# Optimization experiments

Hardware: AMD Instinct MI355X
Metric: run time of the kernel (lower is better)

Reference implementation:

```python
import jax, jax.numpy as jnp
import numpy as np
import math

B, S, D, H = 4, 2048, 1024, 16
DK = D // H


def setup_inputs() -> dict:
    key = jax.random.key(0)
    ks = jax.random.split(key, 12)
    scale = 1.0 / math.sqrt(D)
    inp = {
        "x": jax.random.normal(ks[0], (B, S, D), jnp.float32),
        "q": jax.random.normal(ks[1], (B, S, D), jnp.float32),
        "k": jax.random.normal(ks[2], (B, S, D), jnp.float32),
        "v": jax.random.normal(ks[3], (B, S, D), jnp.float32),
        # causal mask: 1 = keep, 0 = masked
        "mask": jnp.tril(jnp.ones((S, S), jnp.int32))[None, None],
        "wq": jax.random.normal(ks[4], (D, D), jnp.float32) * scale,
        "bq": jnp.zeros((D,), jnp.float32),
        "wk": jax.random.normal(ks[5], (D, D), jnp.float32) * scale,
        "bk": jnp.zeros((D,), jnp.float32),
        "wv": jax.random.normal(ks[6], (D, D), jnp.float32) * scale,
        "bv": jnp.zeros((D,), jnp.float32),
        "wo": jax.random.normal(ks[7], (D, D), jnp.float32) * scale,
        "bo": jnp.zeros((D,), jnp.float32),
    }
    return inp


def _split_heads(t):  # [B,S,D] -> [B,H,S,DK]
    return t.reshape(B, S, H, DK).transpose(0, 2, 1, 3)


def reference(x, q, k, v, mask, wq, bq, wk, bk, wv, bv, wo, bo):
    # x is accepted for signature parity with the torch module but is
    # overwritten inside the original forward; it does not affect output.
    query = _split_heads(q @ wq + bq)
    key_h = _split_heads(k @ wk + bk)
    value = _split_heads(v @ wv + bv)
    # scores: [B,H,Sq,Sk]
    scores = jnp.einsum("bhqd,bhkd->bhqk", query, key_h) / math.sqrt(DK)
    scores = jnp.where(mask == 0, jnp.float32(-1e9), scores)
    attn = jax.nn.softmax(scores, axis=-1)  # dropout p=0.0 -> identity
    out = jnp.einsum("bhqk,bhkd->bhqd", attn, value)
    out = out.transpose(0, 2, 1, 3).reshape(B, S, D)
    return out @ wo + bo
```

## Files before the change

kernel.cpp:

```cpp
#include <hip/hip_runtime.h>

typedef unsigned short u16;
typedef __bf16 bf16x8 __attribute__((ext_vector_type(8)));
typedef float f32x4 __attribute__((ext_vector_type(4)));
typedef u16 u16x8 __attribute__((ext_vector_type(8)));
typedef u16 u16x4 __attribute__((ext_vector_type(4)));

static constexpr int Bb = 4, Ss = 2048, Dd = 1024, Hh = 16, DKk = 64;
static constexpr int Mg = Bb * Ss;
static constexpr int Kg = Dd;
static constexpr int Ng = Dd;

#if __has_builtin(__builtin_amdgcn_exp2f)
#define EXP2 __builtin_amdgcn_exp2f
#else
#define EXP2 exp2f
#endif

__device__ __forceinline__ u16 f2b(float f) {
    union { __bf16 h; u16 u; } c; c.h = (__bf16)f; return c.u;
}

typedef const __attribute__((address_space(1))) void gas_t;
typedef __attribute__((address_space(3))) void las_t;
__device__ __forceinline__ void gll16(const void* g, void* l) {
    __builtin_amdgcn_global_load_lds((gas_t*)g, (las_t*)l, 16, 0, 0);
}

__global__ __launch_bounds__(256) void wt4_kernel(const float* w0, const float* w1,
                                                  const float* w2, const float* w3,
                                                  u16* t0, u16* t1, u16* t2, u16* t3) {
    const float* W; u16* Wt;
    switch (blockIdx.z) {
        case 0: W = w0; Wt = t0; break;
        case 1: W = w1; Wt = t1; break;
        case 2: W = w2; Wt = t2; break;
        default: W = w3; Wt = t3; break;
    }
    __shared__ __attribute__((aligned(16))) u16 T[64 * 72];
    const int k0 = blockIdx.x * 64, n0 = blockIdx.y * 64;
    const int tid = threadIdx.x;
    for (int i = 0; i < 4; ++i) {
        int flat = tid + i * 256;
        int r = flat >> 4, c4 = flat & 15;
        float4 w4 = *(const float4*)(W + (size_t)(k0 + r) * 1024 + n0 + c4 * 4);
        u16* d = &T[r * 72 + c4 * 4];
        d[0] = f2b(w4.x); d[1] = f2b(w4.y); d[2] = f2b(w4.z); d[3] = f2b(w4.w);
    }
    __syncthreads();
    for (int i = 0; i < 2; ++i) {
        int flat = tid + i * 256;
        int n = flat >> 3, c8 = flat & 7;
        u16x8 v;
        for (int jj = 0; jj < 8; ++jj) v[jj] = T[(c8 * 8 + jj) * 72 + n];
        *(u16x8*)(Wt + (size_t)(n0 + n) * 1024 + k0 + c8 * 8) = v;
    }
}

__global__ __launch_bounds__(256) void qkv_gemm(
    const float* __restrict__ qin, const float* __restrict__ kin,
    const float* __restrict__ vin,
    const u16* __restrict__ WqT, const u16* __restrict__ WkT,
    const u16* __restrict__ WvT,
    const float* __restrict__ bq, const float* __restrict__ bk,
    const float* __restrict__ bv,
    u16* __restrict__ Qw, u16* __restrict__ Kw, u16* __restrict__ VwT,
    float qscale) {
    __shared__ __attribute__((aligned(16))) u16 As[128 * 32];
    __shared__ __attribute__((aligned(16))) u16 Bs[128 * 32];
    const int z = blockIdx.z;
    const float* A = (z == 0) ? qin : (z == 1) ? kin : vin;
    const u16* Bt = (z == 0) ? WqT : (z == 1) ? WkT : WvT;
    const float* bias = (z == 0) ? bq : (z == 1) ? bk : bv;
    const float scale = (z == 0) ? qscale : 1.0f;

    const int tid = threadIdx.x;
    const int wave = tid >> 6, lane = tid & 63;
    const int quad = lane >> 4, l15 = lane & 15;
    const int m0 = blockIdx.x * 128, n0 = blockIdx.y * 128;
    const int wm = (wave >> 1) * 64, wn = (wave & 1) * 64;
    const int rr = lane >> 2, cc = (lane & 3) * 8;

    const u16* Bg = Bt + (size_t)(n0 + wave * 32 + rr) * Kg + cc;
    u16* Bsw = &Bs[wave * 32 * 32];

    f32x4 acc[4][4] = {};

    for (int k0 = 0; k0 < Kg; k0 += 32) {
        __syncthreads();
        gll16(Bg + k0, Bsw);
        gll16(Bg + k0 + (size_t)16 * Kg, Bsw + 16 * 32);
        for (int i = 0; i < 4; ++i) {
            int flat = tid + i * 256;
            int r = flat >> 3, c4 = flat & 7;
            float4 a4 = *(const float4*)(A + (size_t)(m0 + r) * Kg + k0 + c4 * 4);
            u16x4 pk;
            pk[0] = f2b(a4.x); pk[1] = f2b(a4.y); pk[2] = f2b(a4.z); pk[3] = f2b(a4.w);
            *(u16x4*)(&As[r * 32 + c4 * 4]) = pk;
        }
        __syncthreads();

        bf16x8 a[4], b[4];
        for (int i = 0; i < 4; ++i)
            a[i] = *(const bf16x8*)(&As[(wm + i * 16 + l15) * 32 + quad * 8]);
        for (int j = 0; j < 4; ++j)
            b[j] = *(const bf16x8*)(&Bs[(wn + j * 16 + l15) * 32 + quad * 8]);
        if (z < 2) {
            for (int i = 0; i < 4; ++i)
                for (int j = 0; j < 4; ++j)
                    acc[i][j] = __builtin_amdgcn_mfma_f32_16x16x32_bf16(b[j], a[i], acc[i][j], 0, 0, 0);
        } else {
            for (int i = 0; i < 4; ++i)
                for (int j = 0; j < 4; ++j)
                    acc[i][j] = __builtin_amdgcn_mfma_f32_16x16x32_bf16(a[i], b[j], acc[i][j], 0, 0, 0);
        }
    }

    if (z < 2) {
        u16* Out = (z == 0) ? Qw : Kw;
        for (int i = 0; i < 4; ++i) {
            int m_row = m0 + wm + i * 16 + l15;
            int bb = m_row >> 11, s = m_row & 2047;
            for (int j = 0; j < 4; ++j) {
                int nb = n0 + wn + j * 16 + quad * 4;
                float4 b4 = *(const float4*)(bias + nb);
                int h = nb >> 6, dk = nb & 63;
                u16x4 pk;
                pk[0] = f2b((acc[i][j][0] + b4.x) * scale);
                pk[1] = f2b((acc[i][j][1] + b4.y) * scale);
                pk[2] = f2b((acc[i][j][2] + b4.z) * scale);
                pk[3] = f2b((acc[i][j][3] + b4.w) * scale);
                *(u16x4*)(Out + (((size_t)bb * Hh + h) * Ss + s) * DKk + dk) = pk;
            }
        }
    } else {
        for (int i = 0; i < 4; ++i) {
            for (int j = 0; j < 4; ++j) {
                int col = n0 + wn + j * 16 + l15;
                float bvv = bias[col];
                int h = col >> 6, dk = col & 63;
                int row0 = m0 + wm + i * 16 + quad * 4;
                int bb = row0 >> 11, s0 = row0 & 2047;
                u16x4 pk;
                for (int r = 0; r < 4; ++r) pk[r] = f2b(acc[i][j][r] + bvv);
                *(u16x4*)(VwT + (((size_t)bb * Hh + h) * DKk + dk) * Ss + s0) = pk;
            }
        }
    }
}

__global__ __launch_bounds__(256) void out_gemm(const u16* __restrict__ A,
                                                const u16* __restrict__ Bt,
                                                const float* __restrict__ bias,
                                                float* __restrict__ Out) {
    __shared__ __attribute__((aligned(16))) u16 As[128 * 32];
    __shared__ __attribute__((aligned(16))) u16 Bs[128 * 32];
    const int tid = threadIdx.x;
    const int wave = tid >> 6, lane = tid & 63;
    const int quad = lane >> 4, l15 = lane & 15;
    const int m0 = blockIdx.x * 128, n0 = blockIdx.y * 128;
    const int wm = (wave >> 1) * 64, wn = (wave & 1) * 64;
    const int rr = lane >> 2, cc = (lane & 3) * 8;

    const u16* Ag = A + (size_t)(m0 + wave * 32 + rr) * Kg + cc;
    const u16* Bg = Bt + (size_t)(n0 + wave * 32 + rr) * Kg + cc;
    u16* Asw = &As[wave * 32 * 32];
    u16* Bsw = &Bs[wave * 32 * 32];

    f32x4 acc[4][4] = {};

    for (int k0 = 0; k0 < Kg; k0 += 32) {
        __syncthreads();
        gll16(Ag + k0, Asw);
        gll16(Ag + k0 + (size_t)16 * Kg, Asw + 16 * 32);
        gll16(Bg + k0, Bsw);
        gll16(Bg + k0 + (size_t)16 * Kg, Bsw + 16 * 32);
        __syncthreads();

        bf16x8 a[4], b[4];
        for (int i = 0; i < 4; ++i)
            a[i] = *(const bf16x8*)(&As[(wm + i * 16 + l15) * 32 + quad * 8]);
        for (int j = 0; j < 4; ++j)
            b[j] = *(const bf16x8*)(&Bs[(wn + j * 16 + l15) * 32 + quad * 8]);
        for (int i = 0; i < 4; ++i)
            for (int j = 0; j < 4; ++j)
                acc[i][j] = __builtin_amdgcn_mfma_f32_16x16x32_bf16(b[j], a[i], acc[i][j], 0, 0, 0);
    }

    for (int i = 0; i < 4; ++i) {
        int m_row = m0 + wm + i * 16 + l15;
        for (int j = 0; j < 4; ++j) {
            int nb = n0 + wn + j * 16 + quad * 4;
            float4 b4 = *(const float4*)(bias + nb);
            float4 o;
            o.x = acc[i][j][0] + b4.x;
            o.y = acc[i][j][1] + b4.y;
            o.z = acc[i][j][2] + b4.z;
            o.w = acc[i][j][3] + b4.w;
            *(float4*)(Out + (size_t)m_row * Ng + nb) = o;
        }
    }
}

__device__ __forceinline__ void tile_step(const u16* Ks, const u16* Vs, u16* Pw,
                                          bf16x8 aq0, bf16x8 aq1, int qrow,
                                          bool diag, int jbase, int quad, int l15,
                                          f32x4 (&acc_o)[4], float& l_r) {
    f32x4 sacc[4];
    for (int ct = 0; ct < 4; ++ct) {
        bf16x8 bk0 = *(const bf16x8*)(&Ks[(ct * 16 + l15) * 32 + quad * 8]);
        bf16x8 bk1 = *(const bf16x8*)(&Ks[2048 + (ct * 16 + l15) * 32 + quad * 8]);
        f32x4 z = {};
        z = __builtin_amdgcn_mfma_f32_16x16x32_bf16(bk0, aq0, z, 0, 0, 0);
        z = __builtin_amdgcn_mfma_f32_16x16x32_bf16(bk1, aq1, z, 0, 0, 0);
        sacc[ct] = z;
    }
    if (diag) {
        for (int ct = 0; ct < 4; ++ct) {
            int kbase = jbase + ct * 16 + quad * 4;
            for (int r = 0; r < 4; ++r)
                if (kbase + r > qrow) sacc[ct][r] = -1e30f;
        }
    }
    const float M0 = 8.0f;
    float sum = 0.f;
    for (int ct = 0; ct < 4; ++ct)
        for (int r = 0; r < 4; ++r) {
            float p = EXP2(sacc[ct][r] - M0);
            sacc[ct][r] = p;
            sum += p;
        }
    l_r += sum;
    for (int ct = 0; ct < 4; ++ct) {
        u16x4 pk;
        for (int r = 0; r < 4; ++r) pk[r] = f2b(sacc[ct][r]);
        *(u16x4*)(&Pw[l15 * 72 + ct * 16 + quad * 4]) = pk;
    }
    for (int sc = 0; sc < 2; ++sc) {
        bf16x8 ap = *(const bf16x8*)(&Pw[l15 * 72 + sc * 32 + quad * 8]);
        for (int dt = 0; dt < 4; ++dt) {
            bf16x8 bv = *(const bf16x8*)(&Vs[sc * 2048 + (dt * 16 + l15) * 32 + quad * 8]);
            acc_o[dt] = __builtin_amdgcn_mfma_f32_16x16x32_bf16(bv, ap, acc_o[dt], 0, 0, 0);
        }
    }
}

__global__ __launch_bounds__(256) void attn_kernel(const u16* __restrict__ Qw,
                                                   const u16* __restrict__ Kw,
                                                   const u16* __restrict__ Vt,
                                                   u16* __restrict__ Ow) {
    __shared__ __attribute__((aligned(16))) u16 QPs[4608];
    __shared__ __attribute__((aligned(16))) u16 Ks[4096];
    __shared__ __attribute__((aligned(16))) u16 Vs[4096];

    const int pi = blockIdx.x;
    const int bh = blockIdx.y;
    const int qt_lo = pi, qt_hi = (Ss / 64 - 1) - pi;
    const int tid = threadIdx.x, wave = tid >> 6, lane = tid & 63;
    const int quad = lane >> 4, l15 = lane & 15;
    const int rr = lane >> 2, cc = (lane & 3) * 8;

    const u16* Qb = Qw + (size_t)bh * Ss * DKk;
    const u16* Kb = Kw + (size_t)bh * Ss * DKk;
    const u16* Vb = Vt + (size_t)bh * DKk * Ss;

    for (int kc = 0; kc < 2; ++kc)
        gll16(Qb + (size_t)(qt_hi * 64 + wave * 16 + rr) * DKk + kc * 32 + cc,
              &QPs[kc * 2048 + wave * 16 * 32]);
    __syncthreads();
    bf16x8 aqh0 = *(const bf16x8*)(&QPs[(wave * 16 + l15) * 32 + quad * 8]);
    bf16x8 aqh1 = *(const bf16x8*)(&QPs[2048 + (wave * 16 + l15) * 32 + quad * 8]);
    __syncthreads();
    for (int kc = 0; kc < 2; ++kc)
        gll16(Qb + (size_t)(qt_lo * 64 + wave * 16 + rr) * DKk + kc * 32 + cc,
              &QPs[kc * 2048 + wave * 16 * 32]);
    __syncthreads();
    bf16x8 aql0 = *(const bf16x8*)(&QPs[(wave * 16 + l15) * 32 + quad * 8]);
    bf16x8 aql1 = *(const bf16x8*)(&QPs[2048 + (wave * 16 + l15) * 32 + quad * 8]);

    f32x4 oh[4] = {}, ol[4] = {};
    float lh = 0.f, ll = 0.f;
    const int qrow_hi = qt_hi * 64 + wave * 16 + l15;
    const int qrow_lo = qt_lo * 64 + wave * 16 + l15;
    u16* Pw = &QPs[wave * 1152];

    for (int j = 0; j <= qt_hi; ++j) {
        __syncthreads();
        for (int c = 0; c < 2; ++c) {
            gll16(Kb + (size_t)(j * 64 + wave * 16 + rr) * DKk + c * 32 + cc,
                  &Ks[c * 2048 + wave * 16 * 32]);
            gll16(Vb + (size_t)(wave * 16 + rr) * Ss + j * 64 + c * 32 + cc,
                  &Vs[c * 2048 + wave * 16 * 32]);
        }
        __syncthreads();

        tile_step(Ks, Vs, Pw, aqh0, aqh1, qrow_hi, j == qt_hi, j * 64, quad, l15, oh, lh);
        if (j <= qt_lo)
            tile_step(Ks, Vs, Pw, aql0, aql1, qrow_lo, j == qt_lo, j * 64, quad, l15, ol, ll);
    }

    const int b = bh >> 4, h = bh & 15;
    {
        float L = lh;
        L += __shfl_xor(L, 16, 64);
        L += __shfl_xor(L, 32, 64);
        float inv = 1.f / L;
        int s = qt_hi * 64 + wave * 16 + l15;
        u16* orow = Ow + (((size_t)b * Ss + s) * Hh + h) * DKk;
        for (int dt = 0; dt < 4; ++dt) {
            u16x4 pk;
            for (int r = 0; r < 4; ++r) pk[r] = f2b(oh[dt][r] * inv);
            *(u16x4*)(orow + dt * 16 + quad * 4) = pk;
        }
    }
    {
        float L = ll;
        L += __shfl_xor(L, 16, 64);
        L += __shfl_xor(L, 32, 64);
        float inv = 1.f / L;
        int s = qt_lo * 64 + wave * 16 + l15;
        u16* orow = Ow + (((size_t)b * Ss + s) * Hh + h) * DKk;
        for (int dt = 0; dt < 4; ++dt) {
            u16x4 pk;
            for (int r = 0; r < 4; ++r) pk[r] = f2b(ol[dt][r] * inv);
            *(u16x4*)(orow + dt * 16 + quad * 4) = pk;
        }
    }
}

extern "C" void kernel_launch(void* const* d_in, const int* in_sizes, int n_in,
                              void* d_out, int out_size, void* d_ws, size_t ws_size,
                              hipStream_t stream) {
    const float* q  = (const float*)d_in[1];
    const float* k  = (const float*)d_in[2];
    const float* v  = (const float*)d_in[3];
    const float* wq = (const float*)d_in[5];
    const float* bq = (const float*)d_in[6];
    const float* wk = (const float*)d_in[7];
    const float* bk = (const float*)d_in[8];
    const float* wv = (const float*)d_in[9];
    const float* bv = (const float*)d_in[10];
    const float* wo = (const float*)d_in[11];
    const float* bo = (const float*)d_in[12];
    float* out = (float*)d_out;

    u16* WqT = (u16*)d_ws;
    u16* WkT = WqT + 1024 * 1024;
    u16* WvT = WkT + 1024 * 1024;
    u16* WoT = WvT + 1024 * 1024;
    u16* Qw  = WoT + 1024 * 1024;
    u16* Kw  = Qw + (size_t)Mg * Kg;
    u16* VwT = Kw + (size_t)Mg * Kg;
    u16* Ow  = VwT + (size_t)Mg * Kg;

    wt4_kernel<<<dim3(16, 16, 4), 256, 0, stream>>>(wq, wk, wv, wo, WqT, WkT, WvT, WoT);

    const float qscale = 0.125f * 1.44269504f;
    qkv_gemm<<<dim3(Mg / 128, Ng / 128, 3), 256, 0, stream>>>(
        q, k, v, WqT, WkT, WvT, bq, bk, bv, Qw, Kw, VwT, qscale);

    attn_kernel<<<dim3(16, 64), 256, 0, stream>>>(Qw, Kw, VwT, Ow);

    out_gemm<<<dim3(Mg / 128, Ng / 128), 256, 0, stream>>>(Ow, WoT, bo, out);
}
```

Baseline: 423.2 us.

## Pre-convert QKV inputs to bf16 and split attention into per-tile blocks

Adds a separate kernel that converts q/k/v from fp32 to bf16 once, so the QKV GEMM can stream A tiles straight into LDS with global_load_lds instead of converting fp32 in registers on every K step. The attention kernel drops the paired hi/lo query-tile load balancing and instead launches one block per query tile, ordered longest-first, with the softmax step inlined. The extra conversion pass costs an additional read/write of the activations. Ow now aliases the converted-input buffer, which is safe only because the QKV GEMM has finished with it by the time attention writes there.

```diff
diff --git a/kernel.cpp b/kernel.cpp
--- a/kernel.cpp
+++ b/kernel.cpp
@@ -25,6 +25,22 @@
 typedef __attribute__((address_space(3))) void las_t;
 __device__ __forceinline__ void gll16(const void* g, void* l) {
     __builtin_amdgcn_global_load_lds((gas_t*)g, (las_t*)l, 16, 0, 0);
+}
+
+__global__ __launch_bounds__(256) void conv3_kernel(const float* __restrict__ q,
+                                                    const float* __restrict__ k,
+                                                    const float* __restrict__ v,
+                                                    u16* __restrict__ dst) {
+    const size_t per = (size_t)Mg * Kg / 8;
+    size_t id = (size_t)blockIdx.x * 256 + threadIdx.x;
+    size_t t = id / per, off = (id % per) * 8;
+    const float* src = (t == 0) ? q : (t == 1) ? k : v;
+    float4 a = *(const float4*)(src + off);
+    float4 b = *(const float4*)(src + off + 4);
+    u16x8 o;
+    o[0] = f2b(a.x); o[1] = f2b(a.y); o[2] = f2b(a.z); o[3] = f2b(a.w);
+    o[4] = f2b(b.x); o[5] = f2b(b.y); o[6] = f2b(b.z); o[7] = f2b(b.w);
+    *(u16x8*)(dst + t * (size_t)Mg * Kg + off) = o;
 }
 
 __global__ __launch_bounds__(256) void wt4_kernel(const float* w0, const float* w1,
@@ -58,8 +74,7 @@
 }
 
 __global__ __launch_bounds__(256) void qkv_gemm(
-    const float* __restrict__ qin, const float* __restrict__ kin,
-    const float* __restrict__ vin,
+    const u16* __restrict__ Ac,
     const u16* __restrict__ WqT, const u16* __restrict__ WkT,
     const u16* __restrict__ WvT,
     const float* __restrict__ bq, const float* __restrict__ bk,
@@ -69,7 +84,7 @@
     __shared__ __attribute__((aligned(16))) u16 As[128 * 32];
     __shared__ __attribute__((aligned(16))) u16 Bs[128 * 32];
     const int z = blockIdx.z;
-    const float* A = (z == 0) ? qin : (z == 1) ? kin : vin;
+    const u16* A = Ac + (size_t)z * Mg * Kg;
     const u16* Bt = (z == 0) ? WqT : (z == 1) ? WkT : WvT;
     const float* bias = (z == 0) ? bq : (z == 1) ? bk : bv;
     const float scale = (z == 0) ? qscale : 1.0f;
@@ -81,23 +96,19 @@
     const int wm = (wave >> 1) * 64, wn = (wave & 1) * 64;
     const int rr = lane >> 2, cc = (lane & 3) * 8;
 
+    const u16* Ag = A + (size_t)(m0 + wave * 32 + rr) * Kg + cc;
     const u16* Bg = Bt + (size_t)(n0 + wave * 32 + rr) * Kg + cc;
+    u16* Asw = &As[wave * 32 * 32];
     u16* Bsw = &Bs[wave * 32 * 32];
 
     f32x4 acc[4][4] = {};
 
     for (int k0 = 0; k0 < Kg; k0 += 32) {
         __syncthreads();
+        gll16(Ag + k0, Asw);
+        gll16(Ag + k0 + (size_t)16 * Kg, Asw + 16 * 32);
         gll16(Bg + k0, Bsw);
         gll16(Bg + k0 + (size_t)16 * Kg, Bsw + 16 * 32);
-        for (int i = 0; i < 4; ++i) {
-            int flat = tid + i * 256;
-            int r = flat >> 3, c4 = flat & 7;
-            float4 a4 = *(const float4*)(A + (size_t)(m0 + r) * Kg + k0 + c4 * 4);
-            u16x4 pk;
-            pk[0] = f2b(a4.x); pk[1] = f2b(a4.y); pk[2] = f2b(a4.z); pk[3] = f2b(a4.w);
-            *(u16x4*)(&As[r * 32 + c4 * 4]) = pk;
-        }
         __syncthreads();
 
         bf16x8 a[4], b[4];
@@ -202,49 +213,6 @@
     }
 }
 
-__device__ __forceinline__ void tile_step(const u16* Ks, const u16* Vs, u16* Pw,
-                                          bf16x8 aq0, bf16x8 aq1, int qrow,
-                                          bool diag, int jbase, int quad, int l15,
-                                          f32x4 (&acc_o)[4], float& l_r) {
-    f32x4 sacc[4];
-    for (int ct = 0; ct < 4; ++ct) {
-        bf16x8 bk0 = *(const bf16x8*)(&Ks[(ct * 16 + l15) * 32 + quad * 8]);
-        bf16x8 bk1 = *(const bf16x8*)(&Ks[2048 + (ct * 16 + l15) * 32 + quad * 8]);
-        f32x4 z = {};
-        z = __builtin_amdgcn_mfma_f32_16x16x32_bf16(bk0, aq0, z, 0, 0, 0);
-        z = __builtin_amdgcn_mfma_f32_16x16x32_bf16(bk1, aq1, z, 0, 0, 0);
-        sacc[ct] = z;
-    }
-    if (diag) {
-        for (int ct = 0; ct < 4; ++ct) {
-            int kbase = jbase + ct * 16 + quad * 4;
-            for (int r = 0; r < 4; ++r)
-                if (kbase + r > qrow) sacc[ct][r] = -1e30f;
-        }
-    }
-    const float M0 = 8.0f;
-    float sum = 0.f;
-    for (int ct = 0; ct < 4; ++ct)
-        for (int r = 0; r < 4; ++r) {
-            float p = EXP2(sacc[ct][r] - M0);
-            sacc[ct][r] = p;
-            sum += p;
-        }
-    l_r += sum;
-    for (int ct = 0; ct < 4; ++ct) {
-        u16x4 pk;
-        for (int r = 0; r < 4; ++r) pk[r] = f2b(sacc[ct][r]);
-        *(u16x4*)(&Pw[l15 * 72 + ct * 16 + quad * 4]) = pk;
-    }
-    for (int sc = 0; sc < 2; ++sc) {
-        bf16x8 ap = *(const bf16x8*)(&Pw[l15 * 72 + sc * 32 + quad * 8]);
-        for (int dt = 0; dt < 4; ++dt) {
-            bf16x8 bv = *(const bf16x8*)(&Vs[sc * 2048 + (dt * 16 + l15) * 32 + quad * 8]);
-            acc_o[dt] = __builtin_amdgcn_mfma_f32_16x16x32_bf16(bv, ap, acc_o[dt], 0, 0, 0);
-        }
-    }
-}
-
 __global__ __launch_bounds__(256) void attn_kernel(const u16* __restrict__ Qw,
                                                    const u16* __restrict__ Kw,
                                                    const u16* __restrict__ Vt,
@@ -253,9 +221,10 @@
     __shared__ __attribute__((aligned(16))) u16 Ks[4096];
     __shared__ __attribute__((aligned(16))) u16 Vs[4096];
 
-    const int pi = blockIdx.x;
-    const int bh = blockIdx.y;
-    const int qt_lo = pi, qt_hi = (Ss / 64 - 1) - pi;
+    const int idx = blockIdx.x;
+    const int qt = (Ss / 64 - 1) - (idx >> 6);
+    const int bh = idx & 63;
+    const int q0 = qt * 64;
     const int tid = threadIdx.x, wave = tid >> 6, lane = tid & 63;
     const int quad = lane >> 4, l15 = lane & 15;
     const int rr = lane >> 2, cc = (lane & 3) * 8;
@@ -265,26 +234,18 @@
     const u16* Vb = Vt + (size_t)bh * DKk * Ss;
 
     for (int kc = 0; kc < 2; ++kc)
-        gll16(Qb + (size_t)(qt_hi * 64 + wave * 16 + rr) * DKk + kc * 32 + cc,
+        gll16(Qb + (size_t)(q0 + wave * 16 + rr) * DKk + kc * 32 + cc,
               &QPs[kc * 2048 + wave * 16 * 32]);
     __syncthreads();
-    bf16x8 aqh0 = *(const bf16x8*)(&QPs[(wave * 16 + l15) * 32 + quad * 8]);
-    bf16x8 aqh1 = *(const bf16x8*)(&QPs[2048 + (wave * 16 + l15) * 32 + quad * 8]);
-    __syncthreads();
-    for (int kc = 0; kc < 2; ++kc)
-        gll16(Qb + (size_t)(qt_lo * 64 + wave * 16 + rr) * DKk + kc * 32 + cc,
-              &QPs[kc * 2048 + wave * 16 * 32]);
-    __syncthreads();
-    bf16x8 aql0 = *(const bf16x8*)(&QPs[(wave * 16 + l15) * 32 + quad * 8]);
-    bf16x8 aql1 = *(const bf16x8*)(&QPs[2048 + (wave * 16 + l15) * 32 + quad * 8]);
-
-    f32x4 oh[4] = {}, ol[4] = {};
-    float lh = 0.f, ll = 0.f;
-    const int qrow_hi = qt_hi * 64 + wave * 16 + l15;
-    const int qrow_lo = qt_lo * 64 + wave * 16 + l15;
+    bf16x8 aq0 = *(const bf16x8*)(&QPs[(wave * 16 + l15) * 32 + quad * 8]);
+    bf16x8 aq1 = *(const bf16x8*)(&QPs[2048 + (wave * 16 + l15) * 32 + quad * 8]);
+
+    f32x4 acc_o[4] = {};
+    float l_r = 0.f;
+    const int qrow = q0 + wave * 16 + l15;
     u16* Pw = &QPs[wave * 1152];
 
-    for (int j = 0; j <= qt_hi; ++j) {
+    for (int j = 0; j <= qt; ++j) {
         __syncthreads();
         for (int c = 0; c < 2; ++c) {
             gll16(Kb + (size_t)(j * 64 + wave * 16 + rr) * DKk + c * 32 + cc,
@@ -294,37 +255,60 @@
         }
         __syncthreads();
 
-        tile_step(Ks, Vs, Pw, aqh0, aqh1, qrow_hi, j == qt_hi, j * 64, quad, l15, oh, lh);
-        if (j <= qt_lo)
-            tile_step(Ks, Vs, Pw, aql0, aql1, qrow_lo, j == qt_lo, j * 64, quad, l15, ol, ll);
+        f32x4 sacc[4];
+        for (int ct = 0; ct < 4; ++ct) {
+            bf16x8 bk0 = *(const bf16x8*)(&Ks[(ct * 16 + l15) * 32 + quad * 8]);
+            bf16x8 bk1 = *(const bf16x8*)(&Ks[2048 + (ct * 16 + l15) * 32 + quad * 8]);
+            f32x4 z = {};
+            z = __builtin_amdgcn_mfma_f32_16x16x32_bf16(bk0, aq0, z, 0, 0, 0);
+            z = __builtin_amdgcn_mfma_f32_16x16x32_bf16(bk1, aq1, z, 0, 0, 0);
+            sacc[ct] = z;
+        }
+
+        if (j == qt) {
+            for (int ct = 0; ct < 4; ++ct) {
+                int kbase = j * 64 + ct * 16 + quad * 4;
+                for (int r = 0; r < 4; ++r)
+                    if (kbase + r > qrow) sacc[ct][r] = -1e30f;
+            }
+        }
+
+        const float M0 = 8.0f;
+        float sum = 0.f;
+        for (int ct = 0; ct < 4; ++ct)
+            for (int r = 0; r < 4; ++r) {
+                float p = EXP2(sacc[ct][r] - M0);
+                sacc[ct][r] = p;
+                sum += p;
+            }
+        l_r += sum;
+
+        for (int ct = 0; ct < 4; ++ct) {
+            u16x4 pk;
+            for (int r = 0; r < 4; ++r) pk[r] = f2b(sacc[ct][r]);
+            *(u16x4*)(&Pw[l15 * 72 + ct * 16 + quad * 4]) = pk;
+        }
+
+        for (int sc = 0; sc < 2; ++sc) {
+            bf16x8 ap = *(const bf16x8*)(&Pw[l15 * 72 + sc * 32 + quad * 8]);
+            for (int dt = 0; dt < 4; ++dt) {
+                bf16x8 bv = *(const bf16x8*)(&Vs[sc * 2048 + (dt * 16 + l15) * 32 + quad * 8]);
+                acc_o[dt] = __builtin_amdgcn_mfma_f32_16x16x32_bf16(bv, ap, acc_o[dt], 0, 0, 0);
+            }
+        }
     }
 
     const int b = bh >> 4, h = bh & 15;
-    {
-        float L = lh;
-        L += __shfl_xor(L, 16, 64);
-        L += __shfl_xor(L, 32, 64);
-        float inv = 1.f / L;
-        int s = qt_hi * 64 + wave * 16 + l15;
-        u16* orow = Ow + (((size_t)b * Ss + s) * Hh + h) * DKk;
-        for (int dt = 0; dt < 4; ++dt) {
-            u16x4 pk;
-            for (int r = 0; r < 4; ++r) pk[r] = f2b(oh[dt][r] * inv);
-            *(u16x4*)(orow + dt * 16 + quad * 4) = pk;
-        }
-    }
-    {
-        float L = ll;
-        L += __shfl_xor(L, 16, 64);
-        L += __shfl_xor(L, 32, 64);
-        float inv = 1.f / L;
-        int s = qt_lo * 64 + wave * 16 + l15;
-        u16* orow = Ow + (((size_t)b * Ss + s) * Hh + h) * DKk;
-        for (int dt = 0; dt < 4; ++dt) {
-            u16x4 pk;
-            for (int r = 0; r < 4; ++r) pk[r] = f2b(ol[dt][r] * inv);
-            *(u16x4*)(orow + dt * 16 + quad * 4) = pk;
-        }
+    float L = l_r;
+    L += __shfl_xor(L, 16, 64);
+    L += __shfl_xor(L, 32, 64);
+    const float inv = 1.f / L;
+    const int s = q0 + wave * 16 + l15;
+    u16* orow = Ow + (((size_t)b * Ss + s) * Hh + h) * DKk;
+    for (int dt = 0; dt < 4; ++dt) {
+        u16x4 pk;
+        for (int r = 0; r < 4; ++r) pk[r] = f2b(acc_o[dt][r] * inv);
+        *(u16x4*)(orow + dt * 16 + quad * 4) = pk;
     }
 }
 
@@ -348,18 +332,20 @@
     u16* WkT = WqT + 1024 * 1024;
     u16* WvT = WkT + 1024 * 1024;
     u16* WoT = WvT + 1024 * 1024;
-    u16* Qw  = WoT + 1024 * 1024;
+    u16* Ac  = WoT + 1024 * 1024;
+    u16* Qw  = Ac + (size_t)3 * Mg * Kg;
     u16* Kw  = Qw + (size_t)Mg * Kg;
     u16* VwT = Kw + (size_t)Mg * Kg;
-    u16* Ow  = VwT + (size_t)Mg * Kg;
-
+    u16* Ow  = Ac;
+
+    conv3_kernel<<<dim3(3 * (Mg * Kg / 8) / 256), 256, 0, stream>>>(q, k, v, Ac);
     wt4_kernel<<<dim3(16, 16, 4), 256, 0, stream>>>(wq, wk, wv, wo, WqT, WkT, WvT, WoT);
 
     const float qscale = 0.125f * 1.44269504f;
     qkv_gemm<<<dim3(Mg / 128, Ng / 128, 3), 256, 0, stream>>>(
-        q, k, v, WqT, WkT, WvT, bq, bk, bv, Qw, Kw, VwT, qscale);
-
-    attn_kernel<<<dim3(16, 64), 256, 0, stream>>>(Qw, Kw, VwT, Ow);
+        Ac, WqT, WkT, WvT, bq, bk, bv, Qw, Kw, VwT, qscale);
+
+    attn_kernel<<<dim3(2048), 256, 0, stream>>>(Qw, Kw, VwT, Ow);
 
     out_gemm<<<dim3(Mg / 128, Ng / 128), 256, 0, stream>>>(Ow, WoT, bo, out);
 }
```

Result: faster. 354.7 us (-16.2%).
